# Kernel optimization log

Measured on AMD Instinct MI355X. Metric: run time of the kernel, lower is better.

Reference implementation:

```python
import jax, jax.numpy as jnp
import numpy as np

B, L, D, H = 2, 2048, 1024, 16
DH = D // H
EPS = 1e-5


def setup_inputs() -> dict:
    key = jax.random.key(0)
    ks = jax.random.split(key, 8)
    s = 0.02  # realistic init scale for weights
    # causal mask: True where attention is DISALLOWED (masked_fill semantics)
    mask = jnp.triu(jnp.ones((L, L), dtype=bool), k=1)[None, None]  # [1,1,L,L]
    return {
        "x": jax.random.normal(ks[0], (B, L, D), jnp.float32),
        "mask": mask,
        "ln_g": jnp.ones((D,), jnp.float32),
        "ln_b": jnp.zeros((D,), jnp.float32),
        "Wq": jax.random.normal(ks[1], (D, D), jnp.float32) * s,
        "bq": jnp.zeros((D,), jnp.float32),
        "Wk": jax.random.normal(ks[2], (D, D), jnp.float32) * s,
        "bk": jnp.zeros((D,), jnp.float32),
        "Wv": jax.random.normal(ks[3], (D, D), jnp.float32) * s,
        "bv": jnp.zeros((D,), jnp.float32),
        "Wo": jax.random.normal(ks[4], (D, D), jnp.float32) * s,
        "bo": jnp.zeros((D,), jnp.float32),
    }


def _layernorm(x, g, b):
    mu = jnp.mean(x, axis=-1, keepdims=True)
    var = jnp.var(x, axis=-1, keepdims=True)
    return (x - mu) * jax.lax.rsqrt(var + EPS) * g + b


def reference(x, mask, ln_g, ln_b, Wq, bq, Wk, bk, Wv, bv, Wo, bo):
    b, l, d = x.shape
    h = _layernorm(x, ln_g, ln_b)
    # separate Q/K/V linears, split into heads: [b, H, l, DH]
    q = (h @ Wq + bq).reshape(b, l, H, DH).transpose(0, 2, 1, 3)
    k = (h @ Wk + bk).reshape(b, l, H, DH).transpose(0, 2, 1, 3)
    v = (h @ Wv + bv).reshape(b, l, H, DH).transpose(0, 2, 1, 3)
    scale = jnp.asarray(DH, x.dtype) ** -0.5
    # full L x L score matrix (this is exactly what the torch module does)
    w = jnp.einsum("bhqd,bhkd->bhqk", q, k) * scale
    w = jnp.where(mask, -jnp.inf, w)
    w = jax.nn.softmax(w, axis=-1)
    # dropout layers are identity in eval mode
    o = jnp.einsum("bhqk,bhkd->bhqd", w, v)
    o = o.transpose(0, 2, 1, 3).reshape(b, l, d)
    return o @ Wo + bo
```

## Files before the change

### kernel.cpp

```cpp
#include <hip/hip_runtime.h>
#include <hip/hip_bf16.h>


typedef __bf16  bf16x8 __attribute__((ext_vector_type(8)));
typedef __bf16  bf16x4 __attribute__((ext_vector_type(4)));
typedef float   f32x4  __attribute__((ext_vector_type(4)));

#define MFMA16(a, b, c) __builtin_amdgcn_mfma_f32_16x16x32_bf16(a, b, c, 0, 0, 0)

#define LDK 40
#define LDT 72

__global__ __launch_bounds__(256) void ln_kernel(
    const float* __restrict__ x, const float* __restrict__ g,
    const float* __restrict__ bta, __hip_bfloat16* __restrict__ h)
{
    __shared__ float red[8];
    const int row = blockIdx.x, t = threadIdx.x;
    const float* xr = x + (size_t)row * 1024;
    const float4 xv = *(const float4*)(xr + t * 4);
    float s  = xv.x + xv.y + xv.z + xv.w;
    float ss = xv.x * xv.x + xv.y * xv.y + xv.z * xv.z + xv.w * xv.w;
    #pragma unroll
    for (int off = 32; off > 0; off >>= 1) {
        s  += __shfl_down(s, off);
        ss += __shfl_down(ss, off);
    }
    const int lane = t & 63, wave = t >> 6;
    if (lane == 0) { red[wave] = s; red[4 + wave] = ss; }
    __syncthreads();
    const float S  = red[0] + red[1] + red[2] + red[3];
    const float SS = red[4] + red[5] + red[6] + red[7];
    const float mu   = S * (1.0f / 1024.0f);
    const float var  = SS * (1.0f / 1024.0f) - mu * mu;
    const float rstd = rsqrtf(var + 1e-5f);
    const float4 gv = *(const float4*)(g + t * 4);
    const float4 bv = *(const float4*)(bta + t * 4);
    __hip_bfloat16* hr = h + (size_t)row * 1024 + t * 4;
    hr[0] = __float2bfloat16((xv.x - mu) * rstd * gv.x + bv.x);
    hr[1] = __float2bfloat16((xv.y - mu) * rstd * gv.y + bv.y);
    hr[2] = __float2bfloat16((xv.z - mu) * rstd * gv.z + bv.z);
    hr[3] = __float2bfloat16((xv.w - mu) * rstd * gv.w + bv.w);
}

__global__ void transpose_cast_kernel(
    const float* __restrict__ Wq, const float* __restrict__ Wk,
    const float* __restrict__ Wv, const float* __restrict__ Wo,
    __hip_bfloat16* __restrict__ tq, __hip_bfloat16* __restrict__ tk,
    __hip_bfloat16* __restrict__ tv, __hip_bfloat16* __restrict__ to_)
{
    __shared__ float t[32][33];
    const int z = blockIdx.z;
    const float* src = (z == 0) ? Wq : (z == 1) ? Wk : (z == 2) ? Wv : Wo;
    __hip_bfloat16* dst = (z == 0) ? tq : (z == 1) ? tk : (z == 2) ? tv : to_;
    const int n0 = blockIdx.x * 32, k0 = blockIdx.y * 32;
    const int tx = threadIdx.x, ty = threadIdx.y;
    t[ty][tx] = src[(size_t)(k0 + ty) * 1024 + n0 + tx];
    __syncthreads();
    dst[(size_t)(n0 + ty) * 1024 + k0 + tx] = __float2bfloat16(t[tx][ty]);
}

__device__ __forceinline__ void gemm_core_1024(
    const __hip_bfloat16* __restrict__ A, const __hip_bfloat16* __restrict__ Bt,
    int m0, int n0, f32x4 (&acc)[4][4])
{
    __shared__ __align__(16) __hip_bfloat16 sA[128 * LDK];
    __shared__ __align__(16) __hip_bfloat16 sB[128 * LDK];
    const int tid  = threadIdx.x;
    const int wave = tid >> 6, lane = tid & 63;
    const int quad = lane >> 4, l16 = lane & 15;
    const int wm = wave >> 1, wn = wave & 1;

    const f32x4 zero = {0.f, 0.f, 0.f, 0.f};
    #pragma unroll
    for (int i = 0; i < 4; ++i)
        #pragma unroll
        for (int j = 0; j < 4; ++j) acc[i][j] = zero;

    for (int k0 = 0; k0 < 1024; k0 += 32) {
        __syncthreads();
        #pragma unroll
        for (int i = 0; i < 2; ++i) {
            const int chunk = tid + 256 * i;
            const int r = chunk >> 2, c = (chunk & 3) << 3;
            *(int4*)(sA + r * LDK + c) = *(const int4*)(A + (size_t)(m0 + r) * 1024 + k0 + c);
            *(int4*)(sB + r * LDK + c) = *(const int4*)(Bt + (size_t)(n0 + r) * 1024 + k0 + c);
        }
        __syncthreads();
        bf16x8 af[4], bfr[4];
        #pragma unroll
        for (int mt = 0; mt < 4; ++mt)
            af[mt] = *(const bf16x8*)(sA + (wm * 64 + mt * 16 + l16) * LDK + quad * 8);
        #pragma unroll
        for (int nt = 0; nt < 4; ++nt)
            bfr[nt] = *(const bf16x8*)(sB + (wn * 64 + nt * 16 + l16) * LDK + quad * 8);
        #pragma unroll
        for (int mt = 0; mt < 4; ++mt)
            #pragma unroll
            for (int nt = 0; nt < 4; ++nt)
                acc[mt][nt] = MFMA16(af[mt], bfr[nt], acc[mt][nt]);
    }
}

__global__ __launch_bounds__(256) void gemm_qkv_kernel(
    const __hip_bfloat16* __restrict__ h,
    const __hip_bfloat16* __restrict__ wt_base,
    const float* __restrict__ bq, const float* __restrict__ bk,
    const float* __restrict__ bv,
    __hip_bfloat16* __restrict__ qkv_base)
{
    const int z = blockIdx.z;
    const __hip_bfloat16* Bt = wt_base + ((size_t)z << 20);
    const float* bias = (z == 0) ? bq : (z == 1) ? bk : bv;
    __hip_bfloat16* outp = qkv_base + ((size_t)z << 22);
    const float scale = (z == 0) ? 0.125f : 1.0f;

    const int m0 = blockIdx.y * 128, n0 = blockIdx.x * 128;
    f32x4 acc[4][4];
    gemm_core_1024(h, Bt, m0, n0, acc);

    const int lane = threadIdx.x & 63, wave = threadIdx.x >> 6;
    const int quad = lane >> 4, l16 = lane & 15;
    const int wm = wave >> 1, wn = wave & 1;
    #pragma unroll
    for (int mt = 0; mt < 4; ++mt)
        #pragma unroll
        for (int nt = 0; nt < 4; ++nt)
            #pragma unroll
            for (int r = 0; r < 4; ++r) {
                const int gm = m0 + wm * 64 + mt * 16 + quad * 4 + r;
                const int gn = n0 + wn * 64 + nt * 16 + l16;
                const float v = (acc[mt][nt][r] + bias[gn]) * scale;
                const int b = gm >> 11, l = gm & 2047;
                const int hh = gn >> 6, dh = gn & 63;
                if (z == 2) {
                    outp[((((size_t)(b * 16 + hh)) * 64 + dh) << 11) + l] = __float2bfloat16(v);
                } else {
                    outp[(((((size_t)(b * 16 + hh)) << 11) + l) * 64) + dh] = __float2bfloat16(v);
                }
            }
}

__global__ __launch_bounds__(256) void gemm_out_kernel(
    const __hip_bfloat16* __restrict__ o, const __hip_bfloat16* __restrict__ wot,
    const float* __restrict__ bo, float* __restrict__ out)
{
    const int m0 = blockIdx.y * 128, n0 = blockIdx.x * 128;
    f32x4 acc[4][4];
    gemm_core_1024(o, wot, m0, n0, acc);

    const int lane = threadIdx.x & 63, wave = threadIdx.x >> 6;
    const int quad = lane >> 4, l16 = lane & 15;
    const int wm = wave >> 1, wn = wave & 1;
    #pragma unroll
    for (int mt = 0; mt < 4; ++mt)
        #pragma unroll
        for (int nt = 0; nt < 4; ++nt)
            #pragma unroll
            for (int r = 0; r < 4; ++r) {
                const int gm = m0 + wm * 64 + mt * 16 + quad * 4 + r;
                const int gn = n0 + wn * 64 + nt * 16 + l16;
                out[(size_t)gm * 1024 + gn] = acc[mt][nt][r] + bo[gn];
            }
}

__global__ __launch_bounds__(256) void attn_kernel(
    const __hip_bfloat16* __restrict__ Q,
    const __hip_bfloat16* __restrict__ Kg,
    const __hip_bfloat16* __restrict__ Vt,
    __hip_bfloat16* __restrict__ O)
{
    __shared__ __align__(16) __hip_bfloat16 sK[64 * LDT];
    __shared__ __align__(16) __hip_bfloat16 sV[64 * LDT];
    __shared__ __align__(16) __hip_bfloat16 sP[128 * LDT];

    const int tid = threadIdx.x;
    const int wave = tid >> 6, lane = tid & 63;
    const int quad = lane >> 4, l16 = lane & 15;
    const int pi = blockIdx.x, bh = blockIdx.y;
    const int qtA = 31 - pi, qtB = pi;
    const int q0A = qtA * 64, q0B = qtB * 64;

    const __hip_bfloat16* Qp = Q  + (size_t)bh * 2048 * 64;
    const __hip_bfloat16* Kp = Kg + (size_t)bh * 2048 * 64;
    const __hip_bfloat16* Vp = Vt + (size_t)bh * 64 * 2048;

    const int rA = q0A + wave * 16 + l16;
    const int rB = q0B + wave * 16 + l16;
    const bf16x8 aqA0 = *(const bf16x8*)(Qp + (size_t)rA * 64 + quad * 8);
    const bf16x8 aqA1 = *(const bf16x8*)(Qp + (size_t)rA * 64 + 32 + quad * 8);
    const bf16x8 aqB0 = *(const bf16x8*)(Qp + (size_t)rB * 64 + quad * 8);
    const bf16x8 aqB1 = *(const bf16x8*)(Qp + (size_t)rB * 64 + 32 + quad * 8);

    const f32x4 zero = {0.f, 0.f, 0.f, 0.f};
    f32x4 oA[4], oB[4];
    #pragma unroll
    for (int nt = 0; nt < 4; ++nt) { oA[nt] = zero; oB[nt] = zero; }
    float mA = -INFINITY, lA = 0.f, mB = -INFINITY, lB = 0.f;

    __hip_bfloat16* sPA = sP + (wave * 16) * LDT;
    __hip_bfloat16* sPB = sP + ((64 + wave * 16)) * LDT;
    const int qloc = wave * 16 + l16;

    auto softmax_tile = [&](const bf16x8& aq0, const bf16x8& aq1,
                            float& m_run, float& l_run, f32x4* oacc,
                            __hip_bfloat16* sPw, bool diag) {
        f32x4 s[4];
        #pragma unroll
        for (int nt = 0; nt < 4; ++nt) {
            const bf16x8 kf0 = *(const bf16x8*)(sK + (nt * 16 + l16) * LDT + quad * 8);
            const bf16x8 kf1 = *(const bf16x8*)(sK + (nt * 16 + l16) * LDT + 32 + quad * 8);
            f32x4 z = zero;
            z = MFMA16(kf0, aq0, z);
            z = MFMA16(kf1, aq1, z);
            s[nt] = z;
        }
        if (diag) {
            #pragma unroll
            for (int nt = 0; nt < 4; ++nt)
                #pragma unroll
                for (int r = 0; r < 4; ++r)
                    if (nt * 16 + quad * 4 + r > qloc) s[nt][r] = -1e30f;
        }
        float mx = -INFINITY;
        #pragma unroll
        for (int nt = 0; nt < 4; ++nt)
            #pragma unroll
            for (int r = 0; r < 4; ++r) mx = fmaxf(mx, s[nt][r]);
        mx = fmaxf(mx, __shfl_xor(mx, 16));
        mx = fmaxf(mx, __shfl_xor(mx, 32));
        const float mnew = fmaxf(m_run, mx);
        const float alpha = __expf(m_run - mnew);
        m_run = mnew;
        float rs = 0.f;
        #pragma unroll
        for (int nt = 0; nt < 4; ++nt) {
            bf16x4 pk;
            #pragma unroll
            for (int r = 0; r < 4; ++r) {
                const float p = __expf(s[nt][r] - mnew);
                rs += p;
                pk[r] = (__bf16)p;
            }
            *(bf16x4*)(sPw + l16 * LDT + nt * 16 + quad * 4) = pk;
        }
        rs += __shfl_xor(rs, 16);
        rs += __shfl_xor(rs, 32);
        l_run = l_run * alpha + rs;
        #pragma unroll
        for (int r = 0; r < 4; ++r) {
            const float aO = __shfl(alpha, quad * 4 + r);
            oacc[0][r] *= aO; oacc[1][r] *= aO; oacc[2][r] *= aO; oacc[3][r] *= aO;
        }
    };

    for (int kt = 0; kt <= qtA; ++kt) {
        const int k0 = kt * 64;
        __syncthreads();
        #pragma unroll
        for (int i2 = 0; i2 < 2; ++i2) {
            const int chunk = tid + 256 * i2;
            const int r = chunk >> 3, c = (chunk & 7) << 3;
            *(int4*)(sK + r * LDT + c) = *(const int4*)(Kp + (size_t)(k0 + r) * 64 + c);
            *(int4*)(sV + r * LDT + c) = *(const int4*)(Vp + (size_t)r * 2048 + k0 + c);
        }
        __syncthreads();

        const bool bAct = (kt <= qtB);
        softmax_tile(aqA0, aqA1, mA, lA, oA, sPA, kt == qtA);
        if (bAct) softmax_tile(aqB0, aqB1, mB, lB, oB, sPB, kt == qtB);

        const bf16x8 apA0 = *(const bf16x8*)(sPA + l16 * LDT + quad * 8);
        const bf16x8 apA1 = *(const bf16x8*)(sPA + l16 * LDT + 32 + quad * 8);
        bf16x8 apB0, apB1;
        if (bAct) {
            apB0 = *(const bf16x8*)(sPB + l16 * LDT + quad * 8);
            apB1 = *(const bf16x8*)(sPB + l16 * LDT + 32 + quad * 8);
        }
        #pragma unroll
        for (int nt = 0; nt < 4; ++nt) {
            const bf16x8 bv0 = *(const bf16x8*)(sV + (nt * 16 + l16) * LDT + quad * 8);
            const bf16x8 bv1 = *(const bf16x8*)(sV + (nt * 16 + l16) * LDT + 32 + quad * 8);
            oA[nt] = MFMA16(apA0, bv0, oA[nt]);
            oA[nt] = MFMA16(apA1, bv1, oA[nt]);
            if (bAct) {
                oB[nt] = MFMA16(apB0, bv0, oB[nt]);
                oB[nt] = MFMA16(apB1, bv1, oB[nt]);
            }
        }
    }

    const int b = bh >> 4, hh = bh & 15;
    #pragma unroll
    for (int t2 = 0; t2 < 2; ++t2) {
        const f32x4* oacc = t2 ? oB : oA;
        const float lrun  = t2 ? lB : lA;
        const int   q0X   = t2 ? q0B : q0A;
        float linv[4];
        #pragma unroll
        for (int r = 0; r < 4; ++r) linv[r] = 1.0f / __shfl(lrun, quad * 4 + r);
        #pragma unroll
        for (int nt = 0; nt < 4; ++nt)
            #pragma unroll
            for (int r = 0; r < 4; ++r) {
                const int qg = q0X + wave * 16 + quad * 4 + r;
                const int dh = nt * 16 + l16;
                O[((size_t)b * 2048 + qg) * 1024 + hh * 64 + dh] =
                    __float2bfloat16(oacc[nt][r] * linv[r]);
            }
    }
}

extern "C" void kernel_launch(void* const* d_in, const int* in_sizes, int n_in,
                              void* d_out, int out_size, void* d_ws, size_t ws_size,
                              hipStream_t stream) {
    const float* x    = (const float*)d_in[0];
    const float* ln_g = (const float*)d_in[2];
    const float* ln_b = (const float*)d_in[3];
    const float* Wq = (const float*)d_in[4];  const float* bq = (const float*)d_in[5];
    const float* Wk = (const float*)d_in[6];  const float* bk = (const float*)d_in[7];
    const float* Wv = (const float*)d_in[8];  const float* bv = (const float*)d_in[9];
    const float* Wo = (const float*)d_in[10]; const float* bo = (const float*)d_in[11];
    float* out = (float*)d_out;

    __hip_bfloat16* ws = (__hip_bfloat16*)d_ws;
    const size_t M1 = 1024 * 1024;
    __hip_bfloat16* h   = ws;
    __hip_bfloat16* wqt = ws + 4 * M1;
    __hip_bfloat16* wot = ws + 7 * M1;
    __hip_bfloat16* q   = ws + 8 * M1;
    __hip_bfloat16* k   = ws + 12 * M1;
    __hip_bfloat16* vt  = ws + 16 * M1;
    __hip_bfloat16* o   = h;

    ln_kernel<<<4096, 256, 0, stream>>>(x, ln_g, ln_b, h);
    transpose_cast_kernel<<<dim3(32, 32, 4), dim3(32, 32), 0, stream>>>(
        Wq, Wk, Wv, Wo, wqt, wqt + M1, wqt + 2 * M1, wot);
    gemm_qkv_kernel<<<dim3(8, 32, 3), 256, 0, stream>>>(h, wqt, bq, bk, bv, q);
    attn_kernel<<<dim3(16, 32), 256, 0, stream>>>(q, k, vt, o);
    gemm_out_kernel<<<dim3(8, 32), 256, 0, stream>>>(o, wot, bo, out);
}
```

Measured before the change: 234.8 us.

## Split paired-tile attention blocks into one query tile per block, use exp2

```diff
diff --git a/kernel.cpp b/kernel.cpp
--- a/kernel.cpp
+++ b/kernel.cpp
@@ -10,6 +10,8 @@
 
 #define LDK 40
 #define LDT 72
+
+#define QSCALE 0.18033688011112042f
 
 __global__ __launch_bounds__(256) void ln_kernel(
     const float* __restrict__ x, const float* __restrict__ g,
@@ -113,7 +115,7 @@
     const __hip_bfloat16* Bt = wt_base + ((size_t)z << 20);
     const float* bias = (z == 0) ? bq : (z == 1) ? bk : bv;
     __hip_bfloat16* outp = qkv_base + ((size_t)z << 22);
-    const float scale = (z == 0) ? 0.125f : 1.0f;
+    const float scale = (z == 0) ? QSCALE : 1.0f;
 
     const int m0 = blockIdx.y * 128, n0 = blockIdx.x * 128;
     f32x4 acc[4][4];
@@ -164,7 +166,7 @@
             }
 }
 
-__global__ __launch_bounds__(256) void attn_kernel(
+__global__ __launch_bounds__(256, 5) void attn_kernel(
     const __hip_bfloat16* __restrict__ Q,
     const __hip_bfloat16* __restrict__ Kg,
     const __hip_bfloat16* __restrict__ Vt,
@@ -172,39 +174,43 @@
 {
     __shared__ __align__(16) __hip_bfloat16 sK[64 * LDT];
     __shared__ __align__(16) __hip_bfloat16 sV[64 * LDT];
-    __shared__ __align__(16) __hip_bfloat16 sP[128 * LDT];
+    __shared__ __align__(16) __hip_bfloat16 sP[64 * LDT];
 
     const int tid = threadIdx.x;
     const int wave = tid >> 6, lane = tid & 63;
     const int quad = lane >> 4, l16 = lane & 15;
-    const int pi = blockIdx.x, bh = blockIdx.y;
-    const int qtA = 31 - pi, qtB = pi;
-    const int q0A = qtA * 64, q0B = qtB * 64;
+    const int qt = 31 - blockIdx.x, bh = blockIdx.y;
+    const int q0 = qt * 64;
 
     const __hip_bfloat16* Qp = Q  + (size_t)bh * 2048 * 64;
     const __hip_bfloat16* Kp = Kg + (size_t)bh * 2048 * 64;
     const __hip_bfloat16* Vp = Vt + (size_t)bh * 64 * 2048;
 
-    const int rA = q0A + wave * 16 + l16;
-    const int rB = q0B + wave * 16 + l16;
-    const bf16x8 aqA0 = *(const bf16x8*)(Qp + (size_t)rA * 64 + quad * 8);
-    const bf16x8 aqA1 = *(const bf16x8*)(Qp + (size_t)rA * 64 + 32 + quad * 8);
-    const bf16x8 aqB0 = *(const bf16x8*)(Qp + (size_t)rB * 64 + quad * 8);
-    const bf16x8 aqB1 = *(const bf16x8*)(Qp + (size_t)rB * 64 + 32 + quad * 8);
+    const int qrow = q0 + wave * 16 + l16;
+    const bf16x8 aq0 = *(const bf16x8*)(Qp + (size_t)qrow * 64 + quad * 8);
+    const bf16x8 aq1 = *(const bf16x8*)(Qp + (size_t)qrow * 64 + 32 + quad * 8);
 
     const f32x4 zero = {0.f, 0.f, 0.f, 0.f};
-    f32x4 oA[4], oB[4];
-    #pragma unroll
-    for (int nt = 0; nt < 4; ++nt) { oA[nt] = zero; oB[nt] = zero; }
-    float mA = -INFINITY, lA = 0.f, mB = -INFINITY, lB = 0.f;
-
-    __hip_bfloat16* sPA = sP + (wave * 16) * LDT;
-    __hip_bfloat16* sPB = sP + ((64 + wave * 16)) * LDT;
+    f32x4 oacc[4];
+    #pragma unroll
+    for (int nt = 0; nt < 4; ++nt) oacc[nt] = zero;
+    float m_run = -INFINITY, l_run = 0.f;
+
+    __hip_bfloat16* sPw = sP + (wave * 16) * LDT;
     const int qloc = wave * 16 + l16;
 
-    auto softmax_tile = [&](const bf16x8& aq0, const bf16x8& aq1,
-                            float& m_run, float& l_run, f32x4* oacc,
-                            __hip_bfloat16* sPw, bool diag) {
+    for (int kt = 0; kt <= qt; ++kt) {
+        const int k0 = kt * 64;
+        __syncthreads();
+        #pragma unroll
+        for (int i2 = 0; i2 < 2; ++i2) {
+            const int chunk = tid + 256 * i2;
+            const int r = chunk >> 3, c = (chunk & 7) << 3;
+            *(int4*)(sK + r * LDT + c) = *(const int4*)(Kp + (size_t)(k0 + r) * 64 + c);
+            *(int4*)(sV + r * LDT + c) = *(const int4*)(Vp + (size_t)r * 2048 + k0 + c);
+        }
+        __syncthreads();
+
         f32x4 s[4];
         #pragma unroll
         for (int nt = 0; nt < 4; ++nt) {
@@ -215,7 +221,7 @@
             z = MFMA16(kf1, aq1, z);
             s[nt] = z;
         }
-        if (diag) {
+        if (kt == qt) {
             #pragma unroll
             for (int nt = 0; nt < 4; ++nt)
                 #pragma unroll
@@ -230,7 +236,7 @@
         mx = fmaxf(mx, __shfl_xor(mx, 16));
         mx = fmaxf(mx, __shfl_xor(mx, 32));
         const float mnew = fmaxf(m_run, mx);
-        const float alpha = __expf(m_run - mnew);
+        const float alpha = exp2f(m_run - mnew);
         m_run = mnew;
         float rs = 0.f;
         #pragma unroll
@@ -238,7 +244,7 @@
             bf16x4 pk;
             #pragma unroll
             for (int r = 0; r < 4; ++r) {
-                const float p = __expf(s[nt][r] - mnew);
+                const float p = exp2f(s[nt][r] - mnew);
                 rs += p;
                 pk[r] = (__bf16)p;
             }
@@ -252,63 +258,31 @@
             const float aO = __shfl(alpha, quad * 4 + r);
             oacc[0][r] *= aO; oacc[1][r] *= aO; oacc[2][r] *= aO; oacc[3][r] *= aO;
         }
-    };
-
-    for (int kt = 0; kt <= qtA; ++kt) {
-        const int k0 = kt * 64;
-        __syncthreads();
-        #pragma unroll
-        for (int i2 = 0; i2 < 2; ++i2) {
-            const int chunk = tid + 256 * i2;
-            const int r = chunk >> 3, c = (chunk & 7) << 3;
-            *(int4*)(sK + r * LDT + c) = *(const int4*)(Kp + (size_t)(k0 + r) * 64 + c);
-            *(int4*)(sV + r * LDT + c) = *(const int4*)(Vp + (size_t)r * 2048 + k0 + c);
-        }
-        __syncthreads();
-
-        const bool bAct = (kt <= qtB);
-        softmax_tile(aqA0, aqA1, mA, lA, oA, sPA, kt == qtA);
-        if (bAct) softmax_tile(aqB0, aqB1, mB, lB, oB, sPB, kt == qtB);
-
-        const bf16x8 apA0 = *(const bf16x8*)(sPA + l16 * LDT + quad * 8);
-        const bf16x8 apA1 = *(const bf16x8*)(sPA + l16 * LDT + 32 + quad * 8);
-        bf16x8 apB0, apB1;
-        if (bAct) {
-            apB0 = *(const bf16x8*)(sPB + l16 * LDT + quad * 8);
-            apB1 = *(const bf16x8*)(sPB + l16 * LDT + 32 + quad * 8);
-        }
+
+        const bf16x8 ap0 = *(const bf16x8*)(sPw + l16 * LDT + quad * 8);
+        const bf16x8 ap1 = *(const bf16x8*)(sPw + l16 * LDT + 32 + quad * 8);
         #pragma unroll
         for (int nt = 0; nt < 4; ++nt) {
             const bf16x8 bv0 = *(const bf16x8*)(sV + (nt * 16 + l16) * LDT + quad * 8);
             const bf16x8 bv1 = *(const bf16x8*)(sV + (nt * 16 + l16) * LDT + 32 + quad * 8);
-            oA[nt] = MFMA16(apA0, bv0, oA[nt]);
-            oA[nt] = MFMA16(apA1, bv1, oA[nt]);
-            if (bAct) {
-                oB[nt] = MFMA16(apB0, bv0, oB[nt]);
-                oB[nt] = MFMA16(apB1, bv1, oB[nt]);
-            }
+            oacc[nt] = MFMA16(ap0, bv0, oacc[nt]);
+            oacc[nt] = MFMA16(ap1, bv1, oacc[nt]);
         }
     }
 
     const int b = bh >> 4, hh = bh & 15;
-    #pragma unroll
-    for (int t2 = 0; t2 < 2; ++t2) {
-        const f32x4* oacc = t2 ? oB : oA;
-        const float lrun  = t2 ? lB : lA;
-        const int   q0X   = t2 ? q0B : q0A;
-        float linv[4];
-        #pragma unroll
-        for (int r = 0; r < 4; ++r) linv[r] = 1.0f / __shfl(lrun, quad * 4 + r);
-        #pragma unroll
-        for (int nt = 0; nt < 4; ++nt)
-            #pragma unroll
-            for (int r = 0; r < 4; ++r) {
-                const int qg = q0X + wave * 16 + quad * 4 + r;
-                const int dh = nt * 16 + l16;
-                O[((size_t)b * 2048 + qg) * 1024 + hh * 64 + dh] =
-                    __float2bfloat16(oacc[nt][r] * linv[r]);
-            }
-    }
+    float linv[4];
+    #pragma unroll
+    for (int r = 0; r < 4; ++r) linv[r] = 1.0f / __shfl(l_run, quad * 4 + r);
+    #pragma unroll
+    for (int nt = 0; nt < 4; ++nt)
+        #pragma unroll
+        for (int r = 0; r < 4; ++r) {
+            const int qg = q0 + wave * 16 + quad * 4 + r;
+            const int dh = nt * 16 + l16;
+            O[((size_t)b * 2048 + qg) * 1024 + hh * 64 + dh] =
+                __float2bfloat16(oacc[nt][r] * linv[r]);
+        }
 }
 
 extern "C" void kernel_launch(void* const* d_in, const int* in_sizes, int n_in,
@@ -337,6 +311,6 @@
     transpose_cast_kernel<<<dim3(32, 32, 4), dim3(32, 32), 0, stream>>>(
         Wq, Wk, Wv, Wo, wqt, wqt + M1, wqt + 2 * M1, wot);
     gemm_qkv_kernel<<<dim3(8, 32, 3), 256, 0, stream>>>(h, wqt, bq, bk, bv, q);
-    attn_kernel<<<dim3(16, 32), 256, 0, stream>>>(q, k, vt, o);
+    attn_kernel<<<dim3(32, 32), 256, 0, stream>>>(q, k, vt, o);
     gemm_out_kernel<<<dim3(8, 32), 256, 0, stream>>>(o, wot, bo, out);
 }
```

Result: slower. 268.6 us (+14.4%).

## Register-prefetch next tiles in GEMM and attention, use exp2 softmax

Applied to the files above, without the earlier changes.

```diff
diff --git a/kernel.cpp b/kernel.cpp
--- a/kernel.cpp
+++ b/kernel.cpp
@@ -8,8 +8,9 @@
 
 #define MFMA16(a, b, c) __builtin_amdgcn_mfma_f32_16x16x32_bf16(a, b, c, 0, 0, 0)
 
-#define LDK 40
 #define LDT 72
+
+#define QSCALE 0.18033688011112042f
 
 __global__ __launch_bounds__(256) void ln_kernel(
     const float* __restrict__ x, const float* __restrict__ g,
@@ -64,8 +65,8 @@
     const __hip_bfloat16* __restrict__ A, const __hip_bfloat16* __restrict__ Bt,
     int m0, int n0, f32x4 (&acc)[4][4])
 {
-    __shared__ __align__(16) __hip_bfloat16 sA[128 * LDK];
-    __shared__ __align__(16) __hip_bfloat16 sB[128 * LDK];
+    __shared__ __align__(16) __hip_bfloat16 sA[128 * LDT];
+    __shared__ __align__(16) __hip_bfloat16 sB[128 * LDT];
     const int tid  = threadIdx.x;
     const int wave = tid >> 6, lane = tid & 63;
     const int quad = lane >> 4, l16 = lane & 15;
@@ -77,28 +78,46 @@
         #pragma unroll
         for (int j = 0; j < 4; ++j) acc[i][j] = zero;
 
-    for (int k0 = 0; k0 < 1024; k0 += 32) {
+    int4 ra[4], rb[4];
+    #pragma unroll
+    for (int i = 0; i < 4; ++i) {
+        const int chunk = tid + 256 * i, r = chunk >> 3, c = (chunk & 7) << 3;
+        ra[i] = *(const int4*)(A  + (size_t)(m0 + r) * 1024 + c);
+        rb[i] = *(const int4*)(Bt + (size_t)(n0 + r) * 1024 + c);
+    }
+
+    for (int k0 = 0; k0 < 1024; k0 += 64) {
         __syncthreads();
         #pragma unroll
-        for (int i = 0; i < 2; ++i) {
-            const int chunk = tid + 256 * i;
-            const int r = chunk >> 2, c = (chunk & 3) << 3;
-            *(int4*)(sA + r * LDK + c) = *(const int4*)(A + (size_t)(m0 + r) * 1024 + k0 + c);
-            *(int4*)(sB + r * LDK + c) = *(const int4*)(Bt + (size_t)(n0 + r) * 1024 + k0 + c);
+        for (int i = 0; i < 4; ++i) {
+            const int chunk = tid + 256 * i, r = chunk >> 3, c = (chunk & 7) << 3;
+            *(int4*)(sA + r * LDT + c) = ra[i];
+            *(int4*)(sB + r * LDT + c) = rb[i];
         }
         __syncthreads();
-        bf16x8 af[4], bfr[4];
-        #pragma unroll
-        for (int mt = 0; mt < 4; ++mt)
-            af[mt] = *(const bf16x8*)(sA + (wm * 64 + mt * 16 + l16) * LDK + quad * 8);
-        #pragma unroll
-        for (int nt = 0; nt < 4; ++nt)
-            bfr[nt] = *(const bf16x8*)(sB + (wn * 64 + nt * 16 + l16) * LDK + quad * 8);
-        #pragma unroll
-        for (int mt = 0; mt < 4; ++mt)
+        if (k0 < 1024 - 64) {
+            #pragma unroll
+            for (int i = 0; i < 4; ++i) {
+                const int chunk = tid + 256 * i, r = chunk >> 3, c = (chunk & 7) << 3;
+                ra[i] = *(const int4*)(A  + (size_t)(m0 + r) * 1024 + k0 + 64 + c);
+                rb[i] = *(const int4*)(Bt + (size_t)(n0 + r) * 1024 + k0 + 64 + c);
+            }
+        }
+        #pragma unroll
+        for (int ko = 0; ko < 2; ++ko) {
+            bf16x8 af[4], bfr[4];
+            #pragma unroll
+            for (int mt = 0; mt < 4; ++mt)
+                af[mt] = *(const bf16x8*)(sA + (wm * 64 + mt * 16 + l16) * LDT + ko * 32 + quad * 8);
             #pragma unroll
             for (int nt = 0; nt < 4; ++nt)
-                acc[mt][nt] = MFMA16(af[mt], bfr[nt], acc[mt][nt]);
+                bfr[nt] = *(const bf16x8*)(sB + (wn * 64 + nt * 16 + l16) * LDT + ko * 32 + quad * 8);
+            #pragma unroll
+            for (int mt = 0; mt < 4; ++mt)
+                #pragma unroll
+                for (int nt = 0; nt < 4; ++nt)
+                    acc[mt][nt] = MFMA16(af[mt], bfr[nt], acc[mt][nt]);
+        }
     }
 }
 
@@ -113,7 +132,7 @@
     const __hip_bfloat16* Bt = wt_base + ((size_t)z << 20);
     const float* bias = (z == 0) ? bq : (z == 1) ? bk : bv;
     __hip_bfloat16* outp = qkv_base + ((size_t)z << 22);
-    const float scale = (z == 0) ? 0.125f : 1.0f;
+    const float scale = (z == 0) ? QSCALE : 1.0f;
 
     const int m0 = blockIdx.y * 128, n0 = blockIdx.x * 128;
     f32x4 acc[4][4];
@@ -170,8 +189,8 @@
     const __hip_bfloat16* __restrict__ Vt,
     __hip_bfloat16* __restrict__ O)
 {
-    __shared__ __align__(16) __hip_bfloat16 sK[64 * LDT];
-    __shared__ __align__(16) __hip_bfloat16 sV[64 * LDT];
+    __shared__ __align__(16) __hip_bfloat16 sK[2][64 * LDT];
+    __shared__ __align__(16) __hip_bfloat16 sV[2][64 * LDT];
     __shared__ __align__(16) __hip_bfloat16 sP[128 * LDT];
 
     const int tid = threadIdx.x;
@@ -199,17 +218,32 @@
     float mA = -INFINITY, lA = 0.f, mB = -INFINITY, lB = 0.f;
 
     __hip_bfloat16* sPA = sP + (wave * 16) * LDT;
-    __hip_bfloat16* sPB = sP + ((64 + wave * 16)) * LDT;
+    __hip_bfloat16* sPB = sP + (64 + wave * 16) * LDT;
     const int qloc = wave * 16 + l16;
 
-    auto softmax_tile = [&](const bf16x8& aq0, const bf16x8& aq1,
+    const int st_r = tid >> 3,        st_c = (tid & 7) << 3;
+    const int st_r1 = (tid + 256) >> 3, st_c1 = ((tid + 256) & 7) << 3;
+
+    int4 rKv[2], rVv[2];
+    rKv[0] = *(const int4*)(Kp + (size_t)st_r  * 64 + st_c);
+    rKv[1] = *(const int4*)(Kp + (size_t)st_r1 * 64 + st_c1);
+    rVv[0] = *(const int4*)(Vp + (size_t)st_r  * 2048 + st_c);
+    rVv[1] = *(const int4*)(Vp + (size_t)st_r1 * 2048 + st_c1);
+    *(int4*)(sK[0] + st_r  * LDT + st_c)  = rKv[0];
+    *(int4*)(sK[0] + st_r1 * LDT + st_c1) = rKv[1];
+    *(int4*)(sV[0] + st_r  * LDT + st_c)  = rVv[0];
+    *(int4*)(sV[0] + st_r1 * LDT + st_c1) = rVv[1];
+    __syncthreads();
+
+    auto softmax_tile = [&](const __hip_bfloat16* sKc,
+                            const bf16x8& aq0, const bf16x8& aq1,
                             float& m_run, float& l_run, f32x4* oacc,
                             __hip_bfloat16* sPw, bool diag) {
         f32x4 s[4];
         #pragma unroll
         for (int nt = 0; nt < 4; ++nt) {
-            const bf16x8 kf0 = *(const bf16x8*)(sK + (nt * 16 + l16) * LDT + quad * 8);
-            const bf16x8 kf1 = *(const bf16x8*)(sK + (nt * 16 + l16) * LDT + 32 + quad * 8);
+            const bf16x8 kf0 = *(const bf16x8*)(sKc + (nt * 16 + l16) * LDT + quad * 8);
+            const bf16x8 kf1 = *(const bf16x8*)(sKc + (nt * 16 + l16) * LDT + 32 + quad * 8);
             f32x4 z = zero;
             z = MFMA16(kf0, aq0, z);
             z = MFMA16(kf1, aq1, z);
@@ -230,7 +264,7 @@
         mx = fmaxf(mx, __shfl_xor(mx, 16));
         mx = fmaxf(mx, __shfl_xor(mx, 32));
         const float mnew = fmaxf(m_run, mx);
-        const float alpha = __expf(m_run - mnew);
+        const float alpha = exp2f(m_run - mnew);
         m_run = mnew;
         float rs = 0.f;
         #pragma unroll
@@ -238,7 +272,7 @@
             bf16x4 pk;
             #pragma unroll
             for (int r = 0; r < 4; ++r) {
-                const float p = __expf(s[nt][r] - mnew);
+                const float p = exp2f(s[nt][r] - mnew);
                 rs += p;
                 pk[r] = (__bf16)p;
             }
@@ -255,20 +289,18 @@
     };
 
     for (int kt = 0; kt <= qtA; ++kt) {
-        const int k0 = kt * 64;
-        __syncthreads();
-        #pragma unroll
-        for (int i2 = 0; i2 < 2; ++i2) {
-            const int chunk = tid + 256 * i2;
-            const int r = chunk >> 3, c = (chunk & 7) << 3;
-            *(int4*)(sK + r * LDT + c) = *(const int4*)(Kp + (size_t)(k0 + r) * 64 + c);
-            *(int4*)(sV + r * LDT + c) = *(const int4*)(Vp + (size_t)r * 2048 + k0 + c);
-        }
-        __syncthreads();
+        const int cur = kt & 1, nxt = cur ^ 1;
+        if (kt < qtA) {
+            const int k0n = (kt + 1) * 64;
+            rKv[0] = *(const int4*)(Kp + (size_t)(k0n + st_r)  * 64 + st_c);
+            rKv[1] = *(const int4*)(Kp + (size_t)(k0n + st_r1) * 64 + st_c1);
+            rVv[0] = *(const int4*)(Vp + (size_t)st_r  * 2048 + k0n + st_c);
+            rVv[1] = *(const int4*)(Vp + (size_t)st_r1 * 2048 + k0n + st_c1);
+        }
 
         const bool bAct = (kt <= qtB);
-        softmax_tile(aqA0, aqA1, mA, lA, oA, sPA, kt == qtA);
-        if (bAct) softmax_tile(aqB0, aqB1, mB, lB, oB, sPB, kt == qtB);
+        softmax_tile(sK[cur], aqA0, aqA1, mA, lA, oA, sPA, kt == qtA);
+        if (bAct) softmax_tile(sK[cur], aqB0, aqB1, mB, lB, oB, sPB, kt == qtB);
 
         const bf16x8 apA0 = *(const bf16x8*)(sPA + l16 * LDT + quad * 8);
         const bf16x8 apA1 = *(const bf16x8*)(sPA + l16 * LDT + 32 + quad * 8);
@@ -279,8 +311,8 @@
         }
         #pragma unroll
         for (int nt = 0; nt < 4; ++nt) {
-            const bf16x8 bv0 = *(const bf16x8*)(sV + (nt * 16 + l16) * LDT + quad * 8);
-            const bf16x8 bv1 = *(const bf16x8*)(sV + (nt * 16 + l16) * LDT + 32 + quad * 8);
+            const bf16x8 bv0 = *(const bf16x8*)(sV[cur] + (nt * 16 + l16) * LDT + quad * 8);
+            const bf16x8 bv1 = *(const bf16x8*)(sV[cur] + (nt * 16 + l16) * LDT + 32 + quad * 8);
             oA[nt] = MFMA16(apA0, bv0, oA[nt]);
             oA[nt] = MFMA16(apA1, bv1, oA[nt]);
             if (bAct) {
@@ -288,6 +320,14 @@
                 oB[nt] = MFMA16(apB1, bv1, oB[nt]);
             }
         }
+
+        if (kt < qtA) {
+            *(int4*)(sK[nxt] + st_r  * LDT + st_c)  = rKv[0];
+            *(int4*)(sK[nxt] + st_r1 * LDT + st_c1) = rKv[1];
+            *(int4*)(sV[nxt] + st_r  * LDT + st_c)  = rVv[0];
+            *(int4*)(sV[nxt] + st_r1 * LDT + st_c1) = rVv[1];
+        }
+        __syncthreads();
     }
 
     const int b = bh >> 4, hh = bh & 15;
```

Result: slower. 368.6 us (+57.0%).

## Use direct global-to-LDS loads in GEMM, swap V GEMM operands, fold log2e into Q scale

Applied to the files above, without the earlier changes.

```diff
diff --git a/kernel.cpp b/kernel.cpp
--- a/kernel.cpp
+++ b/kernel.cpp
@@ -8,8 +8,15 @@
 
 #define MFMA16(a, b, c) __builtin_amdgcn_mfma_f32_16x16x32_bf16(a, b, c, 0, 0, 0)
 
-#define LDK 40
 #define LDT 72
+
+#define QSCALE 0.18033688011112042f
+
+__device__ __forceinline__ void gl_lds16(const void* g, void* l) {
+    __builtin_amdgcn_global_load_lds(
+        (const __attribute__((address_space(1))) void*)g,
+        (__attribute__((address_space(3))) void*)l, 16, 0, 0);
+}
 
 __global__ __launch_bounds__(256) void ln_kernel(
     const float* __restrict__ x, const float* __restrict__ g,
@@ -64,8 +71,8 @@
     const __hip_bfloat16* __restrict__ A, const __hip_bfloat16* __restrict__ Bt,
     int m0, int n0, f32x4 (&acc)[4][4])
 {
-    __shared__ __align__(16) __hip_bfloat16 sA[128 * LDK];
-    __shared__ __align__(16) __hip_bfloat16 sB[128 * LDK];
+    __shared__ __align__(16) __hip_bfloat16 sA[128 * 32];
+    __shared__ __align__(16) __hip_bfloat16 sB[128 * 32];
     const int tid  = threadIdx.x;
     const int wave = tid >> 6, lane = tid & 63;
     const int quad = lane >> 4, l16 = lane & 15;
@@ -77,23 +84,30 @@
         #pragma unroll
         for (int j = 0; j < 4; ++j) acc[i][j] = zero;
 
+    const int r0 = tid >> 2, r1 = 64 + (tid >> 2), cc = (tid & 3) << 3;
+    const __hip_bfloat16* Ap  = A  + (size_t)(m0 + r0) * 1024 + cc;
+    const __hip_bfloat16* Ap1 = A  + (size_t)(m0 + r1) * 1024 + cc;
+    const __hip_bfloat16* Bp  = Bt + (size_t)(n0 + r0) * 1024 + cc;
+    const __hip_bfloat16* Bp1 = Bt + (size_t)(n0 + r1) * 1024 + cc;
+    __hip_bfloat16* lA0 = sA + r0 * 32 + cc;
+    __hip_bfloat16* lA1 = sA + r1 * 32 + cc;
+    __hip_bfloat16* lB0 = sB + r0 * 32 + cc;
+    __hip_bfloat16* lB1 = sB + r1 * 32 + cc;
+
     for (int k0 = 0; k0 < 1024; k0 += 32) {
         __syncthreads();
-        #pragma unroll
-        for (int i = 0; i < 2; ++i) {
-            const int chunk = tid + 256 * i;
-            const int r = chunk >> 2, c = (chunk & 3) << 3;
-            *(int4*)(sA + r * LDK + c) = *(const int4*)(A + (size_t)(m0 + r) * 1024 + k0 + c);
-            *(int4*)(sB + r * LDK + c) = *(const int4*)(Bt + (size_t)(n0 + r) * 1024 + k0 + c);
-        }
+        gl_lds16(Ap  + k0, lA0);
+        gl_lds16(Ap1 + k0, lA1);
+        gl_lds16(Bp  + k0, lB0);
+        gl_lds16(Bp1 + k0, lB1);
         __syncthreads();
         bf16x8 af[4], bfr[4];
         #pragma unroll
         for (int mt = 0; mt < 4; ++mt)
-            af[mt] = *(const bf16x8*)(sA + (wm * 64 + mt * 16 + l16) * LDK + quad * 8);
+            af[mt] = *(const bf16x8*)(sA + (wm * 64 + mt * 16 + l16) * 32 + quad * 8);
         #pragma unroll
         for (int nt = 0; nt < 4; ++nt)
-            bfr[nt] = *(const bf16x8*)(sB + (wn * 64 + nt * 16 + l16) * LDK + quad * 8);
+            bfr[nt] = *(const bf16x8*)(sB + (wn * 64 + nt * 16 + l16) * 32 + quad * 8);
         #pragma unroll
         for (int mt = 0; mt < 4; ++mt)
             #pragma unroll
@@ -110,35 +124,53 @@
     __hip_bfloat16* __restrict__ qkv_base)
 {
     const int z = blockIdx.z;
-    const __hip_bfloat16* Bt = wt_base + ((size_t)z << 20);
-    const float* bias = (z == 0) ? bq : (z == 1) ? bk : bv;
+    const __hip_bfloat16* wt = wt_base + ((size_t)z << 20);
     __hip_bfloat16* outp = qkv_base + ((size_t)z << 22);
-    const float scale = (z == 0) ? 0.125f : 1.0f;
-
-    const int m0 = blockIdx.y * 128, n0 = blockIdx.x * 128;
+
+    const bool swp = (z == 2);
+    const __hip_bfloat16* A  = swp ? wt : h;
+    const __hip_bfloat16* Bt = swp ? h  : wt;
+    const int m0 = swp ? blockIdx.x * 128 : blockIdx.y * 128;
+    const int n0 = swp ? blockIdx.y * 128 : blockIdx.x * 128;
+
     f32x4 acc[4][4];
-    gemm_core_1024(h, Bt, m0, n0, acc);
+    gemm_core_1024(A, Bt, m0, n0, acc);
 
     const int lane = threadIdx.x & 63, wave = threadIdx.x >> 6;
     const int quad = lane >> 4, l16 = lane & 15;
     const int wm = wave >> 1, wn = wave & 1;
-    #pragma unroll
-    for (int mt = 0; mt < 4; ++mt)
-        #pragma unroll
-        for (int nt = 0; nt < 4; ++nt)
-            #pragma unroll
-            for (int r = 0; r < 4; ++r) {
-                const int gm = m0 + wm * 64 + mt * 16 + quad * 4 + r;
-                const int gn = n0 + wn * 64 + nt * 16 + l16;
-                const float v = (acc[mt][nt][r] + bias[gn]) * scale;
-                const int b = gm >> 11, l = gm & 2047;
-                const int hh = gn >> 6, dh = gn & 63;
-                if (z == 2) {
-                    outp[((((size_t)(b * 16 + hh)) * 64 + dh) << 11) + l] = __float2bfloat16(v);
-                } else {
+
+    if (!swp) {
+        const float* bias = (z == 0) ? bq : bk;
+        const float scale = (z == 0) ? QSCALE : 1.0f;
+        #pragma unroll
+        for (int mt = 0; mt < 4; ++mt)
+            #pragma unroll
+            for (int nt = 0; nt < 4; ++nt)
+                #pragma unroll
+                for (int r = 0; r < 4; ++r) {
+                    const int gm = m0 + wm * 64 + mt * 16 + quad * 4 + r;
+                    const int gn = n0 + wn * 64 + nt * 16 + l16;
+                    const float v = (acc[mt][nt][r] + bias[gn]) * scale;
+                    const int b = gm >> 11, l = gm & 2047;
+                    const int hh = gn >> 6, dh = gn & 63;
                     outp[(((((size_t)(b * 16 + hh)) << 11) + l) * 64) + dh] = __float2bfloat16(v);
                 }
-            }
+    } else {
+        #pragma unroll
+        for (int mt = 0; mt < 4; ++mt)
+            #pragma unroll
+            for (int nt = 0; nt < 4; ++nt)
+                #pragma unroll
+                for (int r = 0; r < 4; ++r) {
+                    const int rr = m0 + wm * 64 + mt * 16 + quad * 4 + r;
+                    const int cc = n0 + wn * 64 + nt * 16 + l16;
+                    const float v = acc[mt][nt][r] + bv[rr];
+                    const int b = cc >> 11, l = cc & 2047;
+                    const int hh = rr >> 6, dh = rr & 63;
+                    outp[((((size_t)(b * 16 + hh)) * 64 + dh) << 11) + l] = __float2bfloat16(v);
+                }
+    }
 }
 
 __global__ __launch_bounds__(256) void gemm_out_kernel(
@@ -199,7 +231,7 @@
     float mA = -INFINITY, lA = 0.f, mB = -INFINITY, lB = 0.f;
 
     __hip_bfloat16* sPA = sP + (wave * 16) * LDT;
-    __hip_bfloat16* sPB = sP + ((64 + wave * 16)) * LDT;
+    __hip_bfloat16* sPB = sP + (64 + wave * 16) * LDT;
     const int qloc = wave * 16 + l16;
 
     auto softmax_tile = [&](const bf16x8& aq0, const bf16x8& aq1,
@@ -230,7 +262,7 @@
         mx = fmaxf(mx, __shfl_xor(mx, 16));
         mx = fmaxf(mx, __shfl_xor(mx, 32));
         const float mnew = fmaxf(m_run, mx);
-        const float alpha = __expf(m_run - mnew);
+        const float alpha = exp2f(m_run - mnew);
         m_run = mnew;
         float rs = 0.f;
         #pragma unroll
@@ -238,7 +270,7 @@
             bf16x4 pk;
             #pragma unroll
             for (int r = 0; r < 4; ++r) {
-                const float p = __expf(s[nt][r] - mnew);
+                const float p = exp2f(s[nt][r] - mnew);
                 rs += p;
                 pk[r] = (__bf16)p;
             }
```

After: 240.0 us. +2.2%, slower.
